# Optimization experiments

Measured on AMD Instinct MI355X. Metric: run time of the kernel, lower is better.

## Reference

```python
import jax, jax.numpy as jnp
import numpy as np

B, T, E = 2, 1024, 256   # batch, context, input_emb_size
D = 64                   # query_key_emb_size
DV = 64                  # output_ebm_size


def setup_inputs() -> dict:
    key = jax.random.key(0)
    ks = jax.random.split(key, 12)
    s_in = 1.0 / np.sqrt(E)
    s_2d = 1.0 / np.sqrt(2 * D)
    s_d = 1.0 / np.sqrt(D)
    return {
        "x":  jax.random.normal(ks[0], (B, T, E), dtype=jnp.float32),
        "Wq": jax.random.uniform(ks[1], (E, D), jnp.float32, -s_in, s_in),
        "bq": jax.random.uniform(ks[2], (D,), jnp.float32, -s_in, s_in),
        "Wk": jax.random.uniform(ks[3], (E, D), jnp.float32, -s_in, s_in),
        "bk": jax.random.uniform(ks[4], (D,), jnp.float32, -s_in, s_in),
        "Wv": jax.random.uniform(ks[5], (E, DV), jnp.float32, -s_in, s_in),
        "bv": jax.random.uniform(ks[6], (DV,), jnp.float32, -s_in, s_in),
        "W1": jax.random.uniform(ks[7], (2 * D, D), jnp.float32, -s_2d, s_2d),
        "b1": jax.random.uniform(ks[8], (D,), jnp.float32, -s_2d, s_2d),
        "W2": jax.random.uniform(ks[9], (D, 1), jnp.float32, -s_d, s_d),
        "b2": jax.random.uniform(ks[10], (1,), jnp.float32, -s_d, s_d),
    }


def reference(x, Wq, bq, Wk, bk, Wv, bv, W1, b1, W2, b2):
    # projections (dropout_p = 0 -> dropouts are identity)
    q = jax.nn.relu(x @ Wq + bq)        # [B,T,D]  (activation applied pre-pairing)
    k = jax.nn.relu(x @ Wk + bk)        # [B,T,D]
    v = x @ Wv + bv                     # [B,T,DV]
    t = x.shape[-2]
    d = q.shape[-1]
    # lnr1(concat[q_i, k_j]) == q_i @ W1[:D] + k_j @ W1[D:] + b1 -- avoids the
    # O(T^2 * 2D) concat tensor the torch code materializes via repeat_interleave.
    qp = q @ W1[:d]                     # [B,T,D]
    kp = k @ W1[d:]                     # [B,T,D]
    h = jax.nn.relu(qp[:, :, None, :] + kp[:, None, :, :] + b1)   # [B,T,T,D]
    scores = jnp.einsum('bqkd,d->bqk', h, W2[:, 0]) + b2[0]       # [B,T,T]
    causal = jnp.tril(jnp.ones((t, t), dtype=bool))
    scores = jnp.where(causal, scores, -jnp.inf)
    weights = jax.nn.softmax(scores, axis=-1)                     # [B,T,T]
    out = jnp.einsum('bqk,bkv->bqv', weights, v)                  # [B,T,DV]
    return out
```

## Files before the change

### kernel.cpp

```cpp
#include <hip/hip_runtime.h>

#define B_SZ   2
#define T_CTX  1024
#define E_IN   256
#define D_QK   64
#define DV_OUT 64
#define NROWS  (B_SZ * T_CTX)
#define RPB    8
#define QT     4
#define CH     128
#define SLOT_F 260
#define NTILE  256
#define MAXSP  8
#define BLKS_PER_B 1152


__global__ __launch_bounds__(512) void proj_kernel(
    const float* __restrict__ x,
    const float* __restrict__ Wq, const float* __restrict__ bq,
    const float* __restrict__ Wk, const float* __restrict__ bk,
    const float* __restrict__ Wv, const float* __restrict__ bv,
    const float* __restrict__ W1, const float* __restrict__ b1,
    float* __restrict__ qpb, float* __restrict__ kpt, float* __restrict__ v)
{
    __shared__ float xs[RPB * E_IN];
    __shared__ float qs[RPB * D_QK];
    __shared__ float ks[RPB * D_QK];
    __shared__ float kps[RPB * D_QK];

    const int row0 = blockIdx.x * RPB;
    const int t    = threadIdx.x;

    *(float4*)&xs[4 * t] = *(const float4*)&x[(size_t)row0 * E_IN + 4 * t];
    __syncthreads();

    const int d = t & 63;
    const int r = t >> 6;
    const float* xrow = &xs[r * E_IN];

    float aq0 = 0.f, aq1 = 0.f, ak0 = 0.f, ak1 = 0.f, av0 = 0.f, av1 = 0.f;
    #pragma unroll 8
    for (int e = 0; e < E_IN; e += 2) {
        float x0 = xrow[e], x1 = xrow[e + 1];
        aq0 += x0 * Wq[(e)     * D_QK   + d];
        aq1 += x1 * Wq[(e + 1) * D_QK   + d];
        ak0 += x0 * Wk[(e)     * D_QK   + d];
        ak1 += x1 * Wk[(e + 1) * D_QK   + d];
        av0 += x0 * Wv[(e)     * DV_OUT + d];
        av1 += x1 * Wv[(e + 1) * DV_OUT + d];
    }
    qs[r * D_QK + d] = fmaxf(aq0 + aq1 + bq[d], 0.f);
    ks[r * D_QK + d] = fmaxf(ak0 + ak1 + bk[d], 0.f);
    v[(size_t)(row0 + r) * DV_OUT + d] = av0 + av1 + bv[d];
    __syncthreads();

    const float* qrow = &qs[r * D_QK];
    const float* krow = &ks[r * D_QK];
    float ap0 = 0.f, ap1 = 0.f, bp0 = 0.f, bp1 = 0.f;
    #pragma unroll 8
    for (int e = 0; e < D_QK; e += 2) {
        ap0 += qrow[e]     * W1[(e)            * D_QK + d];
        ap1 += qrow[e + 1] * W1[(e + 1)        * D_QK + d];
        bp0 += krow[e]     * W1[(D_QK + e)     * D_QK + d];
        bp1 += krow[e + 1] * W1[(D_QK + e + 1) * D_QK + d];
    }
    qpb[(size_t)(row0 + r) * D_QK + d] = ap0 + ap1 + b1[d];
    kps[r * D_QK + d] = bp0 + bp1;
    __syncthreads();

    if (t < D_QK) {
        float4 k0 = make_float4(kps[0 * D_QK + t], kps[1 * D_QK + t],
                                kps[2 * D_QK + t], kps[3 * D_QK + t]);
        float4 k1 = make_float4(kps[4 * D_QK + t], kps[5 * D_QK + t],
                                kps[6 * D_QK + t], kps[7 * D_QK + t]);
        *(float4*)&kpt[(size_t)t * NROWS + row0]     = k0;
        *(float4*)&kpt[(size_t)t * NROWS + row0 + 4] = k1;
    }
}

__global__ __launch_bounds__(128) void attn_kernel(
    const float* __restrict__ qpb, const float* __restrict__ kpt,
    const float* __restrict__ v,
    const float* __restrict__ W2, const float* __restrict__ b2,
    float* __restrict__ pws)
{
    __shared__ float qqT[D_QK][QT];
    __shared__ float w2s[D_QK];
    __shared__ float pT[CH][QT];
    __shared__ float redl[2][QT];
    __shared__ float part[2][QT][DV_OUT];

    int u = blockIdx.x;
    int b = 0;
    if (u >= BLKS_PER_B) { b = 1; u -= BLKS_PER_B; }
    int g = 0;
    while (u >= 16 * (g + 1) * (g + 2)) ++g;
    const int loc   = u - 16 * g * (g + 1);
    const int tidx  = loc / (g + 1);
    const int chunk = loc - tidx * (g + 1);
    const int tile  = 32 * g + tidx;
    const int i0    = tile * QT;
    const int jc    = chunk * CH;

    const int t    = threadIdx.x;
    const int lane = t & 63;
    const int wv   = t >> 6;
    const size_t base = (size_t)b * T_CTX;

    #pragma unroll
    for (int k = t; k < QT * D_QK; k += 128) {
        const int q = k >> 6, d = k & 63;
        qqT[d][q] = qpb[(base + i0 + q) * D_QK + d];
    }
    if (t < D_QK) w2s[t] = W2[t];
    __syncthreads();

    const float bias2 = b2[0];
    const int j = jc + t;
    const float* kb = kpt + base + j;

    float acc[QT];
    #pragma unroll
    for (int q = 0; q < QT; ++q) acc[q] = 0.f;

    #pragma unroll 8
    for (int dd = 0; dd < D_QK; ++dd) {
        float kv  = kb[(size_t)dd * NROWS];
        float4 qa = *(const float4*)&qqT[dd][0];
        float wd  = w2s[dd];
        acc[0] += fmaxf(qa.x + kv, 0.f) * wd;
        acc[1] += fmaxf(qa.y + kv, 0.f) * wd;
        acc[2] += fmaxf(qa.z + kv, 0.f) * wd;
        acc[3] += fmaxf(qa.w + kv, 0.f) * wd;
    }

    const int rel = j - i0;
    float p[QT];
    #pragma unroll
    for (int q = 0; q < QT; ++q)
        p[q] = (rel <= q) ? __expf(bias2 + acc[q]) : 0.f;
    *(float4*)&pT[t][0] = make_float4(p[0], p[1], p[2], p[3]);

    #pragma unroll
    for (int q = 0; q < QT; ++q) {
        float lq = p[q];
        #pragma unroll
        for (int o = 32; o > 0; o >>= 1) lq += __shfl_xor(lq, o, 64);
        if (lane == 0) redl[wv][q] = lq;
    }
    __syncthreads();

    const size_t sb = ((size_t)((b * NTILE + tile) * MAXSP + chunk)) * SLOT_F;
    if (t < QT) pws[sb + t] = redl[0][t] + redl[1][t];

    const int half = lane >> 5;
    const int dp   = (lane & 31) * 2;
    float2 av2[QT];
    #pragma unroll
    for (int q = 0; q < QT; ++q) av2[q] = make_float2(0.f, 0.f);

    const float* vb = v + (base + jc + 64 * wv) * DV_OUT + dp;
    #pragma unroll 8
    for (int jj = 0; jj < 64; jj += 2) {
        const int jl = 64 * wv + jj + half;
        float2 vv2 = *(const float2*)(vb + (size_t)(jj + half) * DV_OUT);
        float4 pj  = *(const float4*)&pT[jl][0];
        av2[0].x += pj.x * vv2.x; av2[0].y += pj.x * vv2.y;
        av2[1].x += pj.y * vv2.x; av2[1].y += pj.y * vv2.y;
        av2[2].x += pj.z * vv2.x; av2[2].y += pj.z * vv2.y;
        av2[3].x += pj.w * vv2.x; av2[3].y += pj.w * vv2.y;
    }
    #pragma unroll
    for (int q = 0; q < QT; ++q) {
        av2[q].x += __shfl_xor(av2[q].x, 32, 64);
        av2[q].y += __shfl_xor(av2[q].y, 32, 64);
    }
    if (half == 0) {
        #pragma unroll
        for (int q = 0; q < QT; ++q)
            *(float2*)&part[wv][q][dp] = av2[q];
    }
    __syncthreads();

    #pragma unroll
    for (int k = t; k < QT * DV_OUT; k += 128)
        pws[sb + QT + k] = part[0][k >> 6][k & 63] + part[1][k >> 6][k & 63];
}

__global__ __launch_bounds__(256) void combine_kernel(
    const float* __restrict__ pws, float* __restrict__ out)
{
    const int blk  = blockIdx.x;
    const int b    = blk >> 8;
    const int tile = blk & 255;
    const int nsp  = (tile >> 5) + 1;
    const size_t sb0 = (size_t)((b * NTILE + tile) * MAXSP) * SLOT_F;

    const int t  = threadIdx.x;
    const int q  = t >> 6;
    const int dv = t & 63;

    float L = 0.f, acc = 0.f;
    for (int s = 0; s < nsp; ++s) {
        const size_t sb = sb0 + (size_t)s * SLOT_F;
        L   += pws[sb + q];
        acc += pws[sb + QT + q * 64 + dv];
    }
    out[((size_t)b * T_CTX + tile * QT + q) * DV_OUT + dv] = acc / L;
}

extern "C" void kernel_launch(void* const* d_in, const int* in_sizes, int n_in,
                              void* d_out, int out_size, void* d_ws, size_t ws_size,
                              hipStream_t stream) {
    const float* x  = (const float*)d_in[0];
    const float* Wq = (const float*)d_in[1];
    const float* bq = (const float*)d_in[2];
    const float* Wk = (const float*)d_in[3];
    const float* bk = (const float*)d_in[4];
    const float* Wv = (const float*)d_in[5];
    const float* bv = (const float*)d_in[6];
    const float* W1 = (const float*)d_in[7];
    const float* b1 = (const float*)d_in[8];
    const float* W2 = (const float*)d_in[9];
    const float* b2 = (const float*)d_in[10];
    float* out = (float*)d_out;

    float* ws  = (float*)d_ws;
    float* qpb = ws;
    float* kpt = ws + (size_t)NROWS * D_QK;
    float* vv  = ws + (size_t)2 * NROWS * D_QK;
    float* pws = ws + (size_t)3 * NROWS * D_QK;

    proj_kernel<<<NROWS / RPB, 512, 0, stream>>>(x, Wq, bq, Wk, bk, Wv, bv,
                                                 W1, b1, qpb, kpt, vv);
    attn_kernel<<<B_SZ * BLKS_PER_B, CH, 0, stream>>>(qpb, kpt, vv, W2, b2,
                                                      pws);
    combine_kernel<<<B_SZ * NTILE, 256, 0, stream>>>(pws, out);
}
```

Measured before the change: 41.88 us.

## Replace split-K partial slots with atomic accumulation and simpler finalize

The attention kernel now adds its per-chunk numerator and denominator partials straight into global accumulators with atomicAdd, replacing the slot buffer that the combine kernel had to gather. The projection kernel zeroes these accumulators and is halved to 4 rows per block (256 threads) so its thread count lines up with one zeroing store per output element. A light elementwise finalize kernel divides accumulator by denominator. This removes the strided gather in the combine step but adds atomic contention (up to 8 chunks per tile) and makes the float summation order nondeterministic.

Result: faster. 40.16 us (-4.1%).

```diff
diff --git a/kernel.cpp b/kernel.cpp
--- a/kernel.cpp
+++ b/kernel.cpp
@@ -6,22 +6,21 @@
 #define D_QK   64
 #define DV_OUT 64
 #define NROWS  (B_SZ * T_CTX)
-#define RPB    8
+#define RPB    4
 #define QT     4
 #define CH     128
-#define SLOT_F 260
 #define NTILE  256
-#define MAXSP  8
 #define BLKS_PER_B 1152
 
 
-__global__ __launch_bounds__(512) void proj_kernel(
+__global__ __launch_bounds__(256) void proj_kernel(
     const float* __restrict__ x,
     const float* __restrict__ Wq, const float* __restrict__ bq,
     const float* __restrict__ Wk, const float* __restrict__ bk,
     const float* __restrict__ Wv, const float* __restrict__ bv,
     const float* __restrict__ W1, const float* __restrict__ b1,
-    float* __restrict__ qpb, float* __restrict__ kpt, float* __restrict__ v)
+    float* __restrict__ qpb, float* __restrict__ kpt, float* __restrict__ v,
+    float* __restrict__ outacc, float* __restrict__ lacc)
 {
     __shared__ float xs[RPB * E_IN];
     __shared__ float qs[RPB * D_QK];
@@ -30,6 +29,9 @@
 
     const int row0 = blockIdx.x * RPB;
     const int t    = threadIdx.x;
+
+    outacc[(size_t)row0 * DV_OUT + t] = 0.f;
+    if (t < RPB) lacc[row0 + t] = 0.f;
 
     *(float4*)&xs[4 * t] = *(const float4*)&x[(size_t)row0 * E_IN + 4 * t];
     __syncthreads();
@@ -69,12 +71,9 @@
     __syncthreads();
 
     if (t < D_QK) {
-        float4 k0 = make_float4(kps[0 * D_QK + t], kps[1 * D_QK + t],
+        float4 kq = make_float4(kps[0 * D_QK + t], kps[1 * D_QK + t],
                                 kps[2 * D_QK + t], kps[3 * D_QK + t]);
-        float4 k1 = make_float4(kps[4 * D_QK + t], kps[5 * D_QK + t],
-                                kps[6 * D_QK + t], kps[7 * D_QK + t]);
-        *(float4*)&kpt[(size_t)t * NROWS + row0]     = k0;
-        *(float4*)&kpt[(size_t)t * NROWS + row0 + 4] = k1;
+        *(float4*)&kpt[(size_t)t * NROWS + row0] = kq;
     }
 }
 
@@ -82,7 +81,7 @@
     const float* __restrict__ qpb, const float* __restrict__ kpt,
     const float* __restrict__ v,
     const float* __restrict__ W2, const float* __restrict__ b2,
-    float* __restrict__ pws)
+    float* __restrict__ outacc, float* __restrict__ lacc)
 {
     __shared__ float qqT[D_QK][QT];
     __shared__ float w2s[D_QK];
@@ -149,9 +148,7 @@
         if (lane == 0) redl[wv][q] = lq;
     }
     __syncthreads();
-
-    const size_t sb = ((size_t)((b * NTILE + tile) * MAXSP + chunk)) * SLOT_F;
-    if (t < QT) pws[sb + t] = redl[0][t] + redl[1][t];
+    if (t < QT) atomicAdd(&lacc[base + i0 + t], redl[0][t] + redl[1][t]);
 
     const int half = lane >> 5;
     const int dp   = (lane & 31) * 2;
@@ -183,30 +180,19 @@
     __syncthreads();
 
     #pragma unroll
-    for (int k = t; k < QT * DV_OUT; k += 128)
-        pws[sb + QT + k] = part[0][k >> 6][k & 63] + part[1][k >> 6][k & 63];
-}
-
-__global__ __launch_bounds__(256) void combine_kernel(
-    const float* __restrict__ pws, float* __restrict__ out)
+    for (int k = t; k < QT * DV_OUT; k += 128) {
+        const int q = k >> 6, dv = k & 63;
+        atomicAdd(&outacc[(base + i0 + q) * DV_OUT + dv],
+                  part[0][q][dv] + part[1][q][dv]);
+    }
+}
+
+__global__ __launch_bounds__(512) void finalize_kernel(
+    const float* __restrict__ outacc, const float* __restrict__ lacc,
+    float* __restrict__ out)
 {
-    const int blk  = blockIdx.x;
-    const int b    = blk >> 8;
-    const int tile = blk & 255;
-    const int nsp  = (tile >> 5) + 1;
-    const size_t sb0 = (size_t)((b * NTILE + tile) * MAXSP) * SLOT_F;
-
-    const int t  = threadIdx.x;
-    const int q  = t >> 6;
-    const int dv = t & 63;
-
-    float L = 0.f, acc = 0.f;
-    for (int s = 0; s < nsp; ++s) {
-        const size_t sb = sb0 + (size_t)s * SLOT_F;
-        L   += pws[sb + q];
-        acc += pws[sb + QT + q * 64 + dv];
-    }
-    out[((size_t)b * T_CTX + tile * QT + q) * DV_OUT + dv] = acc / L;
+    const size_t idx = (size_t)blockIdx.x * 512 + threadIdx.x;
+    out[idx] = outacc[idx] / lacc[idx >> 6];
 }
 
 extern "C" void kernel_launch(void* const* d_in, const int* in_sizes, int n_in,
@@ -225,15 +211,18 @@
     const float* b2 = (const float*)d_in[10];
     float* out = (float*)d_out;
 
-    float* ws  = (float*)d_ws;
-    float* qpb = ws;
-    float* kpt = ws + (size_t)NROWS * D_QK;
-    float* vv  = ws + (size_t)2 * NROWS * D_QK;
-    float* pws = ws + (size_t)3 * NROWS * D_QK;
-
-    proj_kernel<<<NROWS / RPB, 512, 0, stream>>>(x, Wq, bq, Wk, bk, Wv, bv,
-                                                 W1, b1, qpb, kpt, vv);
+    float* ws     = (float*)d_ws;
+    float* qpb    = ws;
+    float* kpt    = ws + (size_t)NROWS * D_QK;
+    float* vv     = ws + (size_t)2 * NROWS * D_QK;
+    float* outacc = ws + (size_t)3 * NROWS * D_QK;
+    float* lacc   = ws + (size_t)4 * NROWS * D_QK;
+
+    proj_kernel<<<NROWS / RPB, 256, 0, stream>>>(x, Wq, bq, Wk, bk, Wv, bv,
+                                                 W1, b1, qpb, kpt, vv,
+                                                 outacc, lacc);
     attn_kernel<<<B_SZ * BLKS_PER_B, CH, 0, stream>>>(qpb, kpt, vv, W2, b2,
-                                                      pws);
-    combine_kernel<<<B_SZ * NTILE, 256, 0, stream>>>(pws, out);
-}
+                                                      outacc, lacc);
+    finalize_kernel<<<(NROWS * DV_OUT) / 512, 512, 0, stream>>>(outacc, lacc,
+                                                                out);
+}
```
